# Performance work log

Hardware: AMD Instinct MI355X
Metric: run time of the kernel (lower is better)

The kernel has to match this reference:

```python
import jax, jax.numpy as jnp
import numpy as np
from jax.tree_util import tree_map

B, T, D = 2, 4096, 1024
C = 512            # chunk_size
P = 16             # n_persistent
H = 2048           # neural-memory hidden
FFN = 4 * D        # ffn_mult * d_model
LR, BETA, ALPHA = 0.01, 0.9, 0.01   # memory lr / momentum / decay
EPS_LN = 1e-5


def _l2norm(x):
    n = jnp.sqrt(jnp.sum(x * x, axis=-1, keepdims=True))
    return x / jnp.maximum(n, 1e-12)


def _ln(x, g, b):
    m = jnp.mean(x, axis=-1, keepdims=True)
    v = jnp.mean((x - m) ** 2, axis=-1, keepdims=True)
    return (x - m) * jax.lax.rsqrt(v + EPS_LN) * g + b


def _mem_mlp(mem, x):
    h = jax.nn.silu(x @ mem['w0'] + mem['b0'])
    return h @ mem['w1'] + mem['b1']


def setup_inputs() -> dict:
    key = jax.random.key(0)
    ks = iter(jax.random.split(key, 32))
    w = lambda *s: jax.random.normal(next(ks), s, jnp.float32) * 0.02
    return dict(
        x=jax.random.normal(next(ks), (B, T, D), jnp.float32),
        wq_ctx=w(D, D), wq=w(D, D), wk=w(D, D), wv=w(D, D),
        w_attn_out=w(D, D), w_gate=w(D, D),
        gate_g=jnp.ones(D), gate_b=jnp.zeros(D),
        n1_g=jnp.ones(D), n1_b=jnp.zeros(D),
        n2_g=jnp.ones(D), n2_b=jnp.zeros(D),
        ffn_w1=w(D, FFN), ffn_b1=jnp.zeros(FFN),
        ffn_w2=w(FFN, D), ffn_b2=jnp.zeros(D),
        pers=w(P, D),
        mem_w0=w(D, H), mem_b0=jnp.zeros(H),
        mem_w1=w(H, D), mem_b1=jnp.zeros(D),
        mem_wk=w(D, D), mem_wv=w(D, D),
    )


def reference(x, wq_ctx, wq, wk, wv, w_attn_out, w_gate, gate_g, gate_b,
              n1_g, n1_b, n2_g, n2_b, ffn_w1, ffn_b1, ffn_w2, ffn_b2,
              pers, mem_w0, mem_b0, mem_w1, mem_b1, mem_wk, mem_wv):
    Bv, Tv, Dv = x.shape
    n_chunks = Tv // C
    scale = Dv ** 0.5
    S = P + 2 * C   # persistent + retrieved-memory tokens + segment
    # prefix-aware causal mask: i attends to j if j < P (persistent prefix) or j <= i
    ii = jnp.arange(S)[:, None]
    jj = jnp.arange(S)[None, :]
    mask = (jj < P) | (jj <= ii)                      # (S, S)

    mem0 = dict(w0=mem_w0, b0=mem_b0, w1=mem_w1, b1=mem_b1)
    mom0 = tree_map(jnp.zeros_like, mem0)

    def attn(seq):                                    # cosine causal attention, single head
        q = _l2norm(seq @ wq) * scale
        k = _l2norm(seq @ wk)
        v = seq @ wv
        scores = jnp.einsum('bqd,bkd->bqk', q, k)
        scores = jnp.where(mask, scores, -jnp.inf)
        a = jax.nn.softmax(scores, axis=-1)
        return jnp.einsum('bqk,bkd->bqd', a, v) @ w_attn_out

    def step(carry, seg):                             # seg: (B, C, D)
        mem, mom = carry
        h = _mem_mlp(mem, _l2norm(seg @ wq_ctx))      # memory retrieval, (B, C, D)
        aug = jnp.concatenate(
            [jnp.broadcast_to(pers, (Bv, P, Dv)), h, seg], axis=1)  # (B, S, D)
        y_aug = aug + attn(_ln(aug, n1_g, n1_b))
        y_t = y_aug[:, P + C:, :]                     # strip persistent, keep last C

        # surprise-gradient memory update with momentum + decay
        kk = y_t @ mem_wk
        vv = y_t @ mem_wv
        loss = lambda m: 0.5 * jnp.sum((_mem_mlp(m, kk) - vv) ** 2) / (Bv * C)
        g = jax.grad(loss)(mem)
        mom = tree_map(lambda m_, g_: BETA * m_ + g_, mom, g)
        mem = tree_map(lambda p_, m_: (1.0 - ALPHA) * p_ - LR * m_, mem, mom)

        mem_out = _mem_mlp(mem, _l2norm(y_t @ wq_ctx))
        gate = jax.nn.sigmoid(_ln(y_t, gate_g, gate_b) @ w_gate)
        o = y_t * gate + mem_out * (1.0 - gate)
        h2 = _ln(o, n2_g, n2_b)
        o = o + (jax.nn.silu(h2 @ ffn_w1 + ffn_b1) @ ffn_w2 + ffn_b2)
        return (mem, mom), o

    x_chunks = x.reshape(Bv, n_chunks, C, Dv).transpose(1, 0, 2, 3)
    _, outs = jax.lax.scan(step, (mem0, mom0), x_chunks)   # (n_chunks, B, C, D)
    return outs.transpose(1, 0, 2, 3).reshape(Bv, Tv, Dv)
```

## Files before the change

kernel.cpp:

```cpp
#include <hip/hip_runtime.h>

#define DD 1024
#define HH 2048
#define TT 4096
#define CC 512
#define PPc 16
#define SB 1040
#define KA 1088
#define FFd 4096
#define NCH 8

typedef _Float16 f16x8 __attribute__((ext_vector_type(8)));
typedef float f32x4 __attribute__((ext_vector_type(4)));

typedef const __attribute__((address_space(1))) _Float16* gas_t;
typedef __attribute__((address_space(3))) _Float16* las_t;

__device__ __forceinline__ void async_cp16(const _Float16* g, _Float16* l) {
    __builtin_amdgcn_global_load_lds((gas_t)g, (las_t)l, 16, 0, 0);
}

template<int N> __device__ __forceinline__ void waitvm() {
    static_assert(N == 0 || N == 2 || N == 3 || N == 4 || N == 6 || N == 8, "unsupported vmcnt");
    if constexpr (N == 0)      asm volatile("s_waitcnt vmcnt(0)" ::: "memory");
    else if constexpr (N == 2) asm volatile("s_waitcnt vmcnt(2)" ::: "memory");
    else if constexpr (N == 3) asm volatile("s_waitcnt vmcnt(3)" ::: "memory");
    else if constexpr (N == 4) asm volatile("s_waitcnt vmcnt(4)" ::: "memory");
    else if constexpr (N == 6) asm volatile("s_waitcnt vmcnt(6)" ::: "memory");
    else                       asm volatile("s_waitcnt vmcnt(8)" ::: "memory");
}
#define BARRIER() asm volatile("s_barrier" ::: "memory")

struct GP {
    const _Float16* A; long bsA;
    const _Float16* Bt; long bsB;
    const float* bias;
    const float* resid; long ldr, bsR;
    const float* aux;   long ldx, bsX;
    float* Cf; long ldc, bsC;
    _Float16* Ch; long ldh, bsH;
    _Float16* Ct; long ldt, bsT;
    float* Mom;
    float* Cf2;
    float s1, s2;
    int M, N, K, act;
};

template<int BM, int BN>
__global__ __launch_bounds__(256) void gemm16(GP g)
{
    constexpr int WM = BM / 2, WN = BN / 2;
    constexpr int FA = WM / 16, FB = WN / 16;
    constexpr int LA = BM / 32, LB = BN / 32;
    constexpr int LL = LA + LB;
    constexpr int APAN = BM * 64, BPAN = BN * 64;
    constexpr int NB = 4;
    __shared__ _Float16 smem[NB * (APAN + BPAN)];
    const int tid = threadIdx.x;

    const int gx = gridDim.x, gy = gridDim.y;
    const int nwg = gx * gy * (int)gridDim.z;
    const int orig = ((int)blockIdx.z * gy + (int)blockIdx.y) * gx + (int)blockIdx.x;
    const int xcd = orig & 7, loc = orig >> 3;
    const int q8 = nwg >> 3, r8 = nwg & 7;
    const int lid = (xcd < r8 ? xcd * (q8 + 1) : r8 * (q8 + 1) + (xcd - r8) * q8) + loc;
    const int bxi = lid % gx;
    const int rem = lid / gx;
    const int byi = rem % gy;
    const int z = rem / gy;

    const int K = g.K;
    const int m0 = byi * BM, n0 = bxi * BN;
    const _Float16* Ab = g.A + (long)z * g.bsA + (long)m0 * K;
    const _Float16* Bb = g.Bt + (long)z * g.bsB + (long)n0 * K;
    const int wave = tid >> 6, lane = tid & 63;
    const int wr = wave >> 1, wc = wave & 1;
    const int fr = lane & 15, kq = lane >> 4;
    const int srow = tid >> 3;
    const int sc8 = (((tid & 7) ^ (srow & 7)) << 3);
    f32x4 acc[FA][FB] = {};

    auto stage = [&](int q, int kk) {
#pragma unroll
        for (int r = 0; r < LA; ++r)
            async_cp16(Ab + (long)(r * 32 + srow) * K + kk + sc8,
                       &smem[q * APAN + r * 2048 + wave * 512]);
#pragma unroll
        for (int r = 0; r < LB; ++r)
            async_cp16(Bb + (long)(r * 32 + srow) * K + kk + sc8,
                       &smem[NB * APAN + q * BPAN + r * 2048 + wave * 512]);
    };

    const int sl0 = ((kq ^ (fr & 7)) << 3);
    const int sl1 = (((4 + kq) ^ (fr & 7)) << 3);

    auto compute = [&](int q) {
        f16x8 af[2][FA], bf[2][FB];
        const int abase = q * APAN;
#pragma unroll
        for (int i = 0; i < FA; ++i) {
            const int ro = (wr * WM + i * 16 + fr) * 64;
            af[0][i] = *(const f16x8*)&smem[abase + ro + sl0];
            af[1][i] = *(const f16x8*)&smem[abase + ro + sl1];
        }
        const int bbase = NB * APAN + q * BPAN;
#pragma unroll
        for (int j = 0; j < FB; ++j) {
            const int ro = (wc * WN + j * 16 + fr) * 64;
            bf[0][j] = *(const f16x8*)&smem[bbase + ro + sl0];
            bf[1][j] = *(const f16x8*)&smem[bbase + ro + sl1];
        }
        __builtin_amdgcn_s_setprio(1);
#pragma unroll
        for (int h = 0; h < 2; ++h)
#pragma unroll
            for (int i = 0; i < FA; ++i)
#pragma unroll
                for (int j = 0; j < FB; ++j)
                    acc[i][j] = __builtin_amdgcn_mfma_f32_16x16x32_f16(af[h][i], bf[h][j], acc[i][j], 0, 0, 0);
        __builtin_amdgcn_s_setprio(0);
    };

    const int nk = K >> 6;
    stage(0, 0); stage(1, 64); stage(2, 128);
    int qc = 0, qs = 3;
    for (int t = 0; t < nk; ++t) {
        if (t + 2 < nk)      waitvm<2 * LL>();
        else if (t + 1 < nk) waitvm<LL>();
        else                 waitvm<0>();
        BARRIER();
        if (t + 3 < nk) stage(qs, (t + 3) << 6);
        compute(qc);
        qc = (qc + 1) & 3;
        qs = (qs + 1) & 3;
    }

#pragma unroll
    for (int i = 0; i < FA; ++i) {
        const int gm0 = m0 + wr * WM + i * 16 + kq * 4;
#pragma unroll
        for (int j = 0; j < FB; ++j) {
            const int gn = n0 + wc * WN + j * 16 + fr;
            if (gn >= g.N) continue;
            if (g.act == 4) {
                const int seg = gn >> 10, gl = gn & 1023;
#pragma unroll
                for (int r = 0; r < 4; ++r) {
                    const int gm = gm0 + r;
                    if (gm >= g.M) continue;
                    const float v = acc[i][j][r];
                    if (seg == 0) g.Ch[(long)gm * 1024 + gl] = (_Float16)v;
                    else if (seg == 1) g.Cf[(long)gm * 1024 + gl] = v;
                    else g.Cf2[(long)gm * 1024 + gl] = v;
                }
            } else {
                const float bv = g.bias ? g.bias[gn] : 0.f;
#pragma unroll
                for (int r = 0; r < 4; ++r) {
                    const int gm = gm0 + r;
                    if (gm >= g.M) continue;
                    const float raw = acc[i][j][r] + bv;
                    float av = raw;
                    if (g.act == 1) av = raw / (1.f + __expf(-raw));
                    else if (g.act == 2) {
                        const float a = g.aux[(long)z * g.bsX + (long)gm * g.ldx + gn];
                        const float s = 1.f / (1.f + __expf(-a));
                        av = raw * (s * (1.f + a * (1.f - s)));
                    }
                    float v = g.s1 * av;
                    if (g.resid) v += g.s2 * g.resid[(long)z * g.bsR + (long)gm * g.ldr + gn];
                    if (g.Cf) g.Cf[(long)z * g.bsC + (long)gm * g.ldc + gn] = (g.act == 1) ? raw : v;
                    if (g.Ch) g.Ch[(long)z * g.bsH + (long)gm * g.ldh + gn] = (_Float16)v;
                    acc[i][j][r] = v;
                }
            }
        }
    }

    if (g.Ct && (g.act != 4 || n0 < 1024)) {
        constexpr int TP = BM + 8;
        __syncthreads();
#pragma unroll
        for (int i = 0; i < FA; ++i) {
            const int lm = wr * WM + i * 16 + kq * 4;
#pragma unroll
            for (int j = 0; j < FB; ++j) {
                const int ln = wc * WN + j * 16 + fr;
#pragma unroll
                for (int r = 0; r < 4; ++r)
                    smem[ln * TP + lm + r] = (_Float16)acc[i][j][r];
            }
        }
        __syncthreads();
        constexpr int TPC = 256 / BN;
        constexpr int SEG = BM / TPC;
        const int ln = tid / TPC, part = tid % TPC;
        const int gn = n0 + ln;
        if (gn < g.N) {
            const int gmb = m0 + part * SEG;
            _Float16* dst = g.Ct + (long)z * g.bsT + (long)gn * g.ldt + gmb;
            const _Float16* src = &smem[ln * TP + part * SEG];
#pragma unroll
            for (int gi = 0; gi < SEG / 8; ++gi)
                if (gmb + gi * 8 < g.M)
                    *(uint4*)(dst + gi * 8) = *(const uint4*)(src + gi * 8);
        }
    }
}

__global__ void momupT_k(const float* __restrict__ dW1, float* __restrict__ mom1,
                         float* __restrict__ w1m, _Float16* __restrict__ w1row,
                         _Float16* __restrict__ w1t,
                         const float* __restrict__ dW0, float* __restrict__ mom0,
                         float* __restrict__ w0m, _Float16* __restrict__ w0t)
{
    __shared__ _Float16 t[64][65];
    const int b = blockIdx.x;
    const int tid = threadIdx.x;
    const float* dW; float* mom; float* wm; _Float16* wrow; _Float16* wT;
    int C, RT, r0, c0;
    if (b < 512) {
        dW = dW1; mom = mom1; wm = w1m; wrow = w1row; wT = w1t;
        C = 1024; RT = 2048;
        r0 = (b >> 4) << 6; c0 = (b & 15) << 6;
    } else {
        const int bb = b - 512;
        dW = dW0; mom = mom0; wm = w0m; wrow = nullptr; wT = w0t;
        C = 2048; RT = 1024;
        r0 = (bb >> 5) << 6; c0 = (bb & 31) << 6;
    }
#pragma unroll
    for (int i = 0; i < 4; ++i) {
        const int f = i * 256 + tid;
        const int rr = f >> 4;
        const int c4 = (f & 15) << 2;
        const long idx = (long)(r0 + rr) * C + c0 + c4;
        const float4 d = *(const float4*)(dW + idx);
        float4 mo = *(const float4*)(mom + idx);
        float4 w  = *(const float4*)(wm + idx);
        mo.x = 0.9f * mo.x + d.x; mo.y = 0.9f * mo.y + d.y;
        mo.z = 0.9f * mo.z + d.z; mo.w = 0.9f * mo.w + d.w;
        w.x = 0.99f * w.x - 0.01f * mo.x; w.y = 0.99f * w.y - 0.01f * mo.y;
        w.z = 0.99f * w.z - 0.01f * mo.z; w.w = 0.99f * w.w - 0.01f * mo.w;
        *(float4*)(mom + idx) = mo;
        *(float4*)(wm + idx) = w;
        const _Float16 h0 = (_Float16)w.x, h1 = (_Float16)w.y,
                       h2 = (_Float16)w.z, h3 = (_Float16)w.w;
        if (wrow) {
            wrow[idx] = h0; wrow[idx + 1] = h1;
            wrow[idx + 2] = h2; wrow[idx + 3] = h3;
        }
        t[rr][c4] = h0; t[rr][c4 + 1] = h1; t[rr][c4 + 2] = h2; t[rr][c4 + 3] = h3;
    }
    __syncthreads();
#pragma unroll
    for (int i = 0; i < 4; ++i) {
        const int f = i * 256 + tid;
        const int cc = f >> 4;
        const int rr4 = (f & 15) << 2;
        ushort4 u;
        u.x = *(const unsigned short*)&t[rr4][cc];
        u.y = *(const unsigned short*)&t[rr4 + 1][cc];
        u.z = *(const unsigned short*)&t[rr4 + 2][cc];
        u.w = *(const unsigned short*)&t[rr4 + 3][cc];
        *(ushort4*)(wT + (long)(c0 + cc) * RT + r0 + rr4) = u;
    }
}

__global__ void cvt_k(const float* __restrict__ in, _Float16* __restrict__ out, long n)
{
    long i = ((long)blockIdx.x * 256 + threadIdx.x) * 4;
    if (i >= n) return;
    const float4 v = *(const float4*)(in + i);
    out[i] = (_Float16)v.x; out[i + 1] = (_Float16)v.y;
    out[i + 2] = (_Float16)v.z; out[i + 3] = (_Float16)v.w;
}

__global__ void cvtT_k(const float* __restrict__ in, _Float16* __restrict__ out, int R, int C)
{
    __shared__ _Float16 t[64][65];
    const int c0 = blockIdx.x * 64, r0 = blockIdx.y * 64;
    const int tid = threadIdx.x;
    for (int i = 0; i < 16; ++i) {
        const int lin = i * 256 + tid;
        const int r = lin >> 6, cc = lin & 63;
        t[r][cc] = (_Float16)in[(long)(r0 + r) * C + c0 + cc];
    }
    __syncthreads();
    for (int i = 0; i < 16; ++i) {
        const int lin = i * 256 + tid;
        const int r2 = lin >> 6, c2 = lin & 63;
        out[(long)(c0 + r2) * R + r0 + c2] = t[c2][r2];
    }
}

__global__ void l2n16s_k(const float* __restrict__ in, long ld,
                         _Float16* __restrict__ out, float scale)
{
    const long row = blockIdx.x;
    const float* p = in + row * ld;
    _Float16* q = out + row * DD;
    const int t = threadIdx.x;
    float e0 = p[t], e1 = p[t + 256], e2 = p[t + 512], e3 = p[t + 768];
    __shared__ float rq[256];
    rq[t] = e0 * e0 + e1 * e1 + e2 * e2 + e3 * e3;
    __syncthreads();
    for (int k = 128; k; k >>= 1) { if (t < k) rq[t] += rq[t + k]; __syncthreads(); }
    const float f = scale / fmaxf(sqrtf(rq[0]), 1e-12f);
    q[t] = (_Float16)(e0 * f); q[t + 256] = (_Float16)(e1 * f);
    q[t + 512] = (_Float16)(e2 * f); q[t + 768] = (_Float16)(e3 * f);
}

__global__ void l2qk_k(const float* __restrict__ qk, _Float16* __restrict__ q16,
                       _Float16* __restrict__ k16)
{
    const int blk = blockIdx.x;
    const float* p; _Float16* o; float scale;
    if (blk < 1024) {
        const int b = blk >> 9, r = blk & 511;
        p = qk + (long)(b * SB + PPc + CC + r) * 2048;
        o = q16 + (long)blk * DD; scale = 32.f;
    } else {
        const int row = blk - 1024;
        p = qk + (long)row * 2048 + 1024;
        o = k16 + (long)row * DD; scale = 1.f;
    }
    const int t = threadIdx.x;
    float e0 = p[t], e1 = p[t + 256], e2 = p[t + 512], e3 = p[t + 768];
    __shared__ float rq[256];
    rq[t] = e0 * e0 + e1 * e1 + e2 * e2 + e3 * e3;
    __syncthreads();
    for (int k = 128; k; k >>= 1) { if (t < k) rq[t] += rq[t + k]; __syncthreads(); }
    const float f = scale / fmaxf(sqrtf(rq[0]), 1e-12f);
    o[t] = (_Float16)(e0 * f); o[t + 256] = (_Float16)(e1 * f);
    o[t + 512] = (_Float16)(e2 * f); o[t + 768] = (_Float16)(e3 * f);
}

__global__ void lnaug_k(const float* __restrict__ x, const float* __restrict__ pers,
                        const float* __restrict__ h, const float* __restrict__ g,
                        const float* __restrict__ b, _Float16* __restrict__ out, int c)
{
    const int row = blockIdx.x;
    const int bb = row / SB, i = row % SB;
    const float* p;
    if (i < PPc) p = pers + (long)i * DD;
    else if (i < PPc + CC) p = h + (long)(bb * CC + i - PPc) * DD;
    else p = x + (long)(bb * TT + c * CC + (i - PPc - CC)) * DD;
    _Float16* q = out + (long)row * DD;
    const int t = threadIdx.x;
    float e0 = p[t], e1 = p[t + 256], e2 = p[t + 512], e3 = p[t + 768];
    __shared__ float rs[256], rq[256];
    rs[t] = e0 + e1 + e2 + e3;
    rq[t] = e0 * e0 + e1 * e1 + e2 * e2 + e3 * e3;
    __syncthreads();
    for (int k = 128; k; k >>= 1) {
        if (t < k) { rs[t] += rs[t + k]; rq[t] += rq[t + k]; }
        __syncthreads();
    }
    const float mean = rs[0] * (1.f / DD);
    const float inv = rsqrtf(rq[0] * (1.f / DD) - mean * mean + 1e-5f);
    q[t]       = (_Float16)((e0 - mean) * inv * g[t]       + b[t]);
    q[t + 256] = (_Float16)((e1 - mean) * inv * g[t + 256] + b[t + 256]);
    q[t + 512] = (_Float16)((e2 - mean) * inv * g[t + 512] + b[t + 512]);
    q[t + 768] = (_Float16)((e3 - mean) * inv * g[t + 768] + b[t + 768]);
}

__global__ void softmax16_k(const float* __restrict__ sc, _Float16* __restrict__ pr)
{
    const int blk = blockIdx.x;
    const int r = blk & 511;
    const int i = PPc + CC + r;
    const float* p = sc + (long)blk * SB;
    _Float16* q = pr + (long)blk * KA;
    const int t = threadIdx.x;
    __shared__ float red[256];
    float mx = -3.0e38f;
    for (int j = t; j < SB; j += 256)
        if (j <= i) mx = fmaxf(mx, p[j]);
    red[t] = mx; __syncthreads();
    for (int k = 128; k; k >>= 1) { if (t < k) red[t] = fmaxf(red[t], red[t + k]); __syncthreads(); }
    mx = red[0]; __syncthreads();
    float sum = 0.f;
    for (int j = t; j < SB; j += 256)
        if (j <= i) sum += __expf(p[j] - mx);
    red[t] = sum; __syncthreads();
    for (int k = 128; k; k >>= 1) { if (t < k) red[t] += red[t + k]; __syncthreads(); }
    const float inv = 1.f / red[0];
    for (int j = t; j < KA; j += 256) {
        float e = 0.f;
        if (j < SB && j <= i) e = __expf(p[j] - mx) * inv;
        q[j] = (_Float16)e;
    }
}

__global__ void gateln2_k(const float* __restrict__ yt, const float* __restrict__ gp,
                          const float* __restrict__ mo, const float* __restrict__ g,
                          const float* __restrict__ b, float* __restrict__ OF,
                          _Float16* __restrict__ o16)
{
    const long row = blockIdx.x;
    const int t = threadIdx.x;
    float e[4];
    __shared__ float rs[256], rq[256];
    float ssum = 0.f, qsum = 0.f;
#pragma unroll
    for (int k = 0; k < 4; ++k) {
        const long idx = row * DD + t + k * 256;
        const float s = 1.f / (1.f + __expf(-gp[idx]));
        e[k] = yt[idx] * s + mo[idx] * (1.f - s);
        OF[idx] = e[k];
        ssum += e[k]; qsum += e[k] * e[k];
    }
    rs[t] = ssum; rq[t] = qsum;
    __syncthreads();
    for (int k = 128; k; k >>= 1) {
        if (t < k) { rs[t] += rs[t + k]; rq[t] += rq[t + k]; }
        __syncthreads();
    }
    const float mean = rs[0] * (1.f / DD);
    const float inv = rsqrtf(rq[0] * (1.f / DD) - mean * mean + 1e-5f);
#pragma unroll
    for (int k = 0; k < 4; ++k) {
        const int cc = t + k * 256;
        o16[row * DD + cc] = (_Float16)((e[k] - mean) * inv * g[cc] + b[cc]);
    }
}

__global__ void tailfuse_k(const _Float16* __restrict__ rT, const _Float16* __restrict__ daT,
                           float* __restrict__ mb0, float* __restrict__ mob0,
                           float* __restrict__ mb1, float* __restrict__ mob1,
                           const float* __restrict__ qmp, _Float16* __restrict__ qm16,
                           const float* __restrict__ ytf, const float* __restrict__ gg,
                           const float* __restrict__ gb, _Float16* __restrict__ gl)
{
    const int blk = blockIdx.x;
    const int t = threadIdx.x;
    __shared__ float rs[256], rq[256];
    if (blk < 3072) {
        const _Float16* p = (blk < 1024) ? rT + (long)blk * 1024
                                         : daT + (long)(blk - 1024) * 1024;
        rs[t] = (float)p[t] + (float)p[t + 256] + (float)p[t + 512] + (float)p[t + 768];
        __syncthreads();
        for (int k = 128; k; k >>= 1) { if (t < k) rs[t] += rs[t + k]; __syncthreads(); }
        if (t == 0) {
            const float d = rs[0];
            if (blk < 1024) {
                const float m = 0.9f * mob1[blk] + d;
                mob1[blk] = m;
                mb1[blk] = 0.99f * mb1[blk] - 0.01f * m;
            } else {
                const int j = blk - 1024;
                const float m = 0.9f * mob0[j] + d;
                mob0[j] = m;
                mb0[j] = 0.99f * mb0[j] - 0.01f * m;
            }
        }
    } else if (blk < 4096) {
        const long row = blk - 3072;
        const float* p = qmp + row * DD;
        _Float16* q = qm16 + row * DD;
        float e0 = p[t], e1 = p[t + 256], e2 = p[t + 512], e3 = p[t + 768];
        rq[t] = e0 * e0 + e1 * e1 + e2 * e2 + e3 * e3;
        __syncthreads();
        for (int k = 128; k; k >>= 1) { if (t < k) rq[t] += rq[t + k]; __syncthreads(); }
        const float f = 1.f / fmaxf(sqrtf(rq[0]), 1e-12f);
        q[t] = (_Float16)(e0 * f); q[t + 256] = (_Float16)(e1 * f);
        q[t + 512] = (_Float16)(e2 * f); q[t + 768] = (_Float16)(e3 * f);
    } else {
        const long row = blk - 4096;
        const float* p = ytf + row * DD;
        _Float16* q = gl + row * DD;
        float e0 = p[t], e1 = p[t + 256], e2 = p[t + 512], e3 = p[t + 768];
        rs[t] = e0 + e1 + e2 + e3;
        rq[t] = e0 * e0 + e1 * e1 + e2 * e2 + e3 * e3;
        __syncthreads();
        for (int k = 128; k; k >>= 1) {
            if (t < k) { rs[t] += rs[t + k]; rq[t] += rq[t + k]; }
            __syncthreads();
        }
        const float mean = rs[0] * (1.f / DD);
        const float inv = rsqrtf(rq[0] * (1.f / DD) - mean * mean + 1e-5f);
        q[t]       = (_Float16)((e0 - mean) * inv * gg[t]       + gb[t]);
        q[t + 256] = (_Float16)((e1 - mean) * inv * gg[t + 256] + gb[t + 256]);
        q[t + 512] = (_Float16)((e2 - mean) * inv * gg[t + 512] + gb[t + 512]);
        q[t + 768] = (_Float16)((e3 - mean) * inv * gg[t + 768] + gb[t + 768]);
    }
}

__global__ void zero_k(float* __restrict__ p, long n)
{
    long i = (long)blockIdx.x * 256 + threadIdx.x;
    const long st = (long)gridDim.x * 256;
    for (; i < n; i += st) p[i] = 0.f;
}

extern "C" void kernel_launch(void* const* d_in, const int* in_sizes, int n_in,
                              void* d_out, int out_size, void* d_ws, size_t ws_size,
                              hipStream_t stream)
{
    const float* x          = (const float*)d_in[0];
    const float* wq_ctx     = (const float*)d_in[1];
    const float* wq         = (const float*)d_in[2];
    const float* wk         = (const float*)d_in[3];
    const float* wv         = (const float*)d_in[4];
    const float* w_attn_out = (const float*)d_in[5];
    const float* w_gate     = (const float*)d_in[6];
    const float* gate_g     = (const float*)d_in[7];
    const float* gate_b     = (const float*)d_in[8];
    const float* n1_g       = (const float*)d_in[9];
    const float* n1_b       = (const float*)d_in[10];
    const float* n2_g       = (const float*)d_in[11];
    const float* n2_b       = (const float*)d_in[12];
    const float* ffn_w1     = (const float*)d_in[13];
    const float* ffn_b1     = (const float*)d_in[14];
    const float* ffn_w2     = (const float*)d_in[15];
    const float* ffn_b2     = (const float*)d_in[16];
    const float* pers       = (const float*)d_in[17];
    const float* mem_w0_in  = (const float*)d_in[18];
    const float* mem_b0_in  = (const float*)d_in[19];
    const float* mem_w1_in  = (const float*)d_in[20];
    const float* mem_b1_in  = (const float*)d_in[21];
    const float* mem_wk     = (const float*)d_in[22];
    const float* mem_wv     = (const float*)d_in[23];
    float* out = (float*)d_out;
    (void)in_sizes; (void)n_in; (void)out_size; (void)ws_size;

    char* cur = (char*)d_ws;
    auto allocF = [&](size_t n) { float* p = (float*)cur; cur += n * 4; return p; };
    auto allocH = [&](size_t n) { _Float16* p = (_Float16*)cur; cur += n * 2; return p; };

    float* mw0   = allocF((size_t)DD * HH);
    float* mw1   = allocF((size_t)HH * DD);
    float* mb0   = allocF(HH);
    float* mb1   = allocF(DD);
    float* mom   = allocF((size_t)DD * HH * 2 + HH + DD);
    float* mom_w0 = mom, *mom_w1 = mom + (size_t)DD * HH;
    float* mom_b0 = mom_w1 + (size_t)HH * DD, *mom_b1 = mom_b0 + HH;
    float* F32A  = allocF((size_t)1024 * DD);
    float* F32B  = allocF((size_t)1024 * DD);
    float* F32C  = allocF((size_t)1024 * HH);
    float* F32QK = allocF((size_t)2112 * 2048);
    float* YTF   = allocF((size_t)1024 * DD);
    float* OF    = allocF((size_t)1024 * DD);

    _Float16* x16    = allocH((size_t)2 * TT * DD);
    _Float16* wqcT   = allocH((size_t)DD * DD);
    _Float16* wqkT   = allocH((size_t)2048 * DD);
    _Float16* wvT    = allocH((size_t)DD * DD);
    _Float16* waoT   = allocH((size_t)DD * DD);
    _Float16* wgT    = allocH((size_t)DD * DD);
    _Float16* wmixT  = allocH((size_t)3072 * DD);
    _Float16* f1T    = allocH((size_t)FFd * DD);
    _Float16* f2T    = allocH((size_t)DD * FFd);
    _Float16* w0T    = allocH((size_t)HH * DD);
    _Float16* w1T    = allocH((size_t)DD * HH);
    _Float16* w1p    = allocH((size_t)HH * DD);
    _Float16* xn16   = allocH((size_t)1024 * DD);
    _Float16* h116   = allocH((size_t)1024 * HH);
    _Float16* laug16 = allocH((size_t)2208 * DD);
    _Float16* q16    = allocH((size_t)1024 * DD);
    _Float16* k16    = allocH((size_t)2208 * DD);
    _Float16* vT16   = allocH((size_t)2 * DD * KA);
    _Float16* pr16   = allocH((size_t)2 * 512 * KA);
    _Float16* ao16   = allocH((size_t)1024 * DD);
    _Float16* yt16   = allocH((size_t)1024 * DD);
    _Float16* kk16   = allocH((size_t)1024 * DD);
    _Float16* kkT16  = allocH((size_t)DD * 1024);
    _Float16* hs16   = allocH((size_t)1024 * HH);
    _Float16* hsT16  = allocH((size_t)HH * 1024);
    _Float16* r16    = allocH((size_t)1024 * DD);
    _Float16* rT16   = allocH((size_t)DD * 1024);
    _Float16* da0T   = allocH((size_t)HH * 1024);
    _Float16* qm16   = allocH((size_t)1024 * DD);
    _Float16* a216   = allocH((size_t)1024 * HH);
    _Float16* gl16   = allocH((size_t)1024 * DD);
    _Float16* h216   = allocH((size_t)1024 * DD);
    _Float16* f116   = allocH((size_t)1024 * FFd);

    auto launch = [&](int nz, const GP& g) {
        dim3 grid((g.N + 63) / 64, (g.M + 63) / 64, nz);
        gemm16<64, 64><<<grid, 256, 0, stream>>>(g);
    };

    hipMemcpyAsync(mw0, mem_w0_in, sizeof(float) * DD * HH, hipMemcpyDeviceToDevice, stream);
    hipMemcpyAsync(mw1, mem_w1_in, sizeof(float) * HH * DD, hipMemcpyDeviceToDevice, stream);
    hipMemcpyAsync(mb0, mem_b0_in, sizeof(float) * HH, hipMemcpyDeviceToDevice, stream);
    hipMemcpyAsync(mb1, mem_b1_in, sizeof(float) * DD, hipMemcpyDeviceToDevice, stream);
    zero_k<<<4096, 256, 0, stream>>>(mom, (long)DD * HH * 2 + HH + DD);
    cvt_k<<<(2 * TT * DD) / 1024, 256, 0, stream>>>(x, x16, (long)2 * TT * DD);
    auto T64 = [&](const float* in, _Float16* o, int R, int C) {
        cvtT_k<<<dim3(C / 64, R / 64), 256, 0, stream>>>(in, o, R, C);
    };
    T64(wq_ctx, wqcT, DD, DD);
    T64(wq, wqkT, DD, DD); T64(wk, wqkT + (size_t)1024 * DD, DD, DD);
    T64(wv, wvT, DD, DD); T64(w_attn_out, waoT, DD, DD); T64(w_gate, wgT, DD, DD);
    T64(mem_wk, wmixT, DD, DD); T64(mem_wv, wmixT + (size_t)1024 * DD, DD, DD);
    T64(wq_ctx, wmixT + (size_t)2048 * DD, DD, DD);
    T64(ffn_w1, f1T, DD, FFd); T64(ffn_w2, f2T, FFd, DD);
    T64(mem_w0_in, w0T, DD, HH); T64(mem_w1_in, w1T, HH, DD);
    cvt_k<<<(HH * DD) / 1024, 256, 0, stream>>>(mem_w1_in, w1p, (long)HH * DD);

    for (int c = 0; c < NCH; ++c) {
        GP g;
        g = GP{}; g.A = x16 + (long)c * CC * DD; g.bsA = (long)TT * DD; g.Bt = wqcT;
        g.Cf = F32A; g.ldc = DD; g.bsC = (long)CC * DD;
        g.s1 = 1.f; g.M = CC; g.N = DD; g.K = DD;
        launch(2, g);
        l2n16s_k<<<1024, 256, 0, stream>>>(F32A, DD, xn16, 1.f);
        g = GP{}; g.A = xn16; g.Bt = w0T; g.bias = mb0; g.Ch = h116; g.ldh = HH;
        g.s1 = 1.f; g.M = 1024; g.N = HH; g.K = DD; g.act = 1;
        launch(1, g);
        g = GP{}; g.A = h116; g.Bt = w1T; g.bias = mb1; g.Cf = F32B; g.ldc = DD;
        g.s1 = 1.f; g.M = 1024; g.N = DD; g.K = HH;
        launch(1, g);
        lnaug_k<<<2 * SB, 256, 0, stream>>>(x, pers, F32B, n1_g, n1_b, laug16, c);
        g = GP{}; g.A = laug16; g.Bt = wqkT; g.Cf = F32QK; g.ldc = 2048;
        g.s1 = 1.f; g.M = 2 * SB; g.N = 2048; g.K = DD;
        launch(1, g);
        l2qk_k<<<3104, 256, 0, stream>>>(F32QK, q16, k16);
        g = GP{}; g.A = laug16; g.bsA = (long)SB * DD; g.Bt = wvT;
        g.Ct = vT16; g.ldt = KA; g.bsT = (long)DD * KA;
        g.s1 = 1.f; g.M = SB; g.N = DD; g.K = DD;
        launch(2, g);
        g = GP{}; g.A = q16; g.bsA = (long)512 * DD; g.Bt = k16; g.bsB = (long)SB * DD;
        g.Cf = F32C; g.ldc = SB; g.bsC = (long)512 * SB;
        g.s1 = 1.f; g.M = 512; g.N = SB; g.K = DD;
        launch(2, g);
        softmax16_k<<<1024, 256, 0, stream>>>(F32C, pr16);
        g = GP{}; g.A = pr16; g.bsA = (long)512 * KA; g.Bt = vT16; g.bsB = (long)DD * KA;
        g.Ch = ao16; g.ldh = DD; g.bsH = (long)512 * DD;
        g.s1 = 1.f; g.M = 512; g.N = DD; g.K = KA;
        launch(2, g);
        g = GP{}; g.A = ao16; g.bsA = (long)512 * DD; g.Bt = waoT;
        g.resid = x + (long)c * CC * DD; g.ldr = DD; g.bsR = (long)TT * DD;
        g.Cf = YTF; g.ldc = DD; g.bsC = (long)512 * DD;
        g.Ch = yt16; g.ldh = DD; g.bsH = (long)512 * DD;
        g.s1 = 1.f; g.s2 = 1.f; g.M = 512; g.N = DD; g.K = DD;
        launch(2, g);
        g = GP{}; g.A = yt16; g.Bt = wmixT; g.Ch = kk16; g.Ct = kkT16; g.ldt = 1024;
        g.Cf = F32B; g.Cf2 = F32A;
        g.s1 = 1.f; g.M = 1024; g.N = 3072; g.K = DD; g.act = 4;
        launch(1, g);
        g = GP{}; g.A = kk16; g.Bt = w0T; g.bias = mb0; g.Cf = F32C; g.ldc = HH;
        g.Ch = hs16; g.ldh = HH; g.Ct = hsT16; g.ldt = 1024;
        g.s1 = 1.f; g.M = 1024; g.N = HH; g.K = DD; g.act = 1;
        launch(1, g);
        g = GP{}; g.A = hs16; g.Bt = w1T; g.bias = mb1;
        g.resid = F32B; g.ldr = DD;
        g.Ch = r16; g.ldh = DD; g.Ct = rT16; g.ldt = 1024;
        g.s1 = 1.f / 1024.f; g.s2 = -1.f / 1024.f; g.M = 1024; g.N = DD; g.K = HH;
        launch(1, g);
        g = GP{}; g.A = r16; g.Bt = w1p; g.aux = F32C; g.ldx = HH;
        g.Ct = da0T; g.ldt = 1024;
        g.s1 = 1.f; g.M = 1024; g.N = HH; g.K = DD; g.act = 2;
        launch(1, g);
        tailfuse_k<<<5120, 256, 0, stream>>>(rT16, da0T, mb0, mom_b0, mb1, mom_b1,
                                             F32A, qm16, YTF, gate_g, gate_b, gl16);
        g = GP{}; g.A = hsT16; g.Bt = rT16; g.Cf = F32C; g.ldc = DD;
        g.s1 = 1.f; g.M = HH; g.N = DD; g.K = 1024;
        launch(1, g);
        g = GP{}; g.A = kkT16; g.Bt = da0T; g.Cf = F32QK; g.ldc = HH;
        g.s1 = 1.f; g.M = DD; g.N = HH; g.K = 1024;
        launch(1, g);
        momupT_k<<<1024, 256, 0, stream>>>(F32C, mom_w1, mw1, w1p, w1T,
                                           F32QK, mom_w0, mw0, w0T);
        g = GP{}; g.A = qm16; g.Bt = w0T; g.bias = mb0; g.Ch = a216; g.ldh = HH;
        g.s1 = 1.f; g.M = 1024; g.N = HH; g.K = DD; g.act = 1;
        launch(1, g);
        g = GP{}; g.A = a216; g.Bt = w1T; g.bias = mb1; g.Cf = F32B; g.ldc = DD;
        g.s1 = 1.f; g.M = 1024; g.N = DD; g.K = HH;
        launch(1, g);
        g = GP{}; g.A = gl16; g.Bt = wgT; g.Cf = F32C; g.ldc = DD;
        g.s1 = 1.f; g.M = 1024; g.N = DD; g.K = DD;
        launch(1, g);
        gateln2_k<<<1024, 256, 0, stream>>>(YTF, F32C, F32B, n2_g, n2_b, OF, h216);
        g = GP{}; g.A = h216; g.Bt = f1T; g.bias = ffn_b1; g.Ch = f116; g.ldh = FFd;
        g.s1 = 1.f; g.M = 1024; g.N = FFd; g.K = DD; g.act = 1;
        launch(1, g);
        g = GP{}; g.A = f116; g.bsA = (long)512 * FFd; g.Bt = f2T; g.bias = ffn_b2;
        g.resid = OF; g.ldr = DD; g.bsR = (long)512 * DD;
        g.Cf = out + (long)c * CC * DD; g.ldc = DD; g.bsC = (long)TT * DD;
        g.s1 = 1.f; g.s2 = 1.f; g.M = 512; g.N = DD; g.K = FFd;
        launch(2, g);
    }
}
```

Measured before the change: 3.272 ms.

## Split-K small GEMMs with reduction fused into consumers, trim GEMM pipeline to 3 stages

Adds leading-dimension fields to the GEMM so K can be split across the z grid dimension. The two memory-MLP second-layer GEMMs (K=2048) and the gate GEMM (K=1024) now run as 2-way split-K into separate scratch buffers. The partial sums and bias are added in the downstream lnaug and gateln2 kernels, which raises occupancy for these 1024x1024 outputs. The GEMM's shared-memory ring also drops from 4 to 3 stages, cutting LDS use and possibly raising occupancy, at the cost of less prefetch depth. It also relies on the F32QK scratch being free at these points in the schedule.

```diff
diff --git a/kernel.cpp b/kernel.cpp
--- a/kernel.cpp
+++ b/kernel.cpp
@@ -32,8 +32,8 @@
 #define BARRIER() asm volatile("s_barrier" ::: "memory")
 
 struct GP {
-    const _Float16* A; long bsA;
-    const _Float16* Bt; long bsB;
+    const _Float16* A; long bsA, ldA;
+    const _Float16* Bt; long bsB, ldB;
     const float* bias;
     const float* resid; long ldr, bsR;
     const float* aux;   long ldx, bsX;
@@ -54,7 +54,7 @@
     constexpr int LA = BM / 32, LB = BN / 32;
     constexpr int LL = LA + LB;
     constexpr int APAN = BM * 64, BPAN = BN * 64;
-    constexpr int NB = 4;
+    constexpr int NB = 3;
     __shared__ _Float16 smem[NB * (APAN + BPAN)];
     const int tid = threadIdx.x;
 
@@ -70,9 +70,10 @@
     const int z = rem / gy;
 
     const int K = g.K;
+    const long ldA = g.ldA, ldB = g.ldB;
     const int m0 = byi * BM, n0 = bxi * BN;
-    const _Float16* Ab = g.A + (long)z * g.bsA + (long)m0 * K;
-    const _Float16* Bb = g.Bt + (long)z * g.bsB + (long)n0 * K;
+    const _Float16* Ab = g.A + (long)z * g.bsA + (long)m0 * ldA;
+    const _Float16* Bb = g.Bt + (long)z * g.bsB + (long)n0 * ldB;
     const int wave = tid >> 6, lane = tid & 63;
     const int wr = wave >> 1, wc = wave & 1;
     const int fr = lane & 15, kq = lane >> 4;
@@ -83,11 +84,11 @@
     auto stage = [&](int q, int kk) {
 #pragma unroll
         for (int r = 0; r < LA; ++r)
-            async_cp16(Ab + (long)(r * 32 + srow) * K + kk + sc8,
+            async_cp16(Ab + (long)(r * 32 + srow) * ldA + kk + sc8,
                        &smem[q * APAN + r * 2048 + wave * 512]);
 #pragma unroll
         for (int r = 0; r < LB; ++r)
-            async_cp16(Bb + (long)(r * 32 + srow) * K + kk + sc8,
+            async_cp16(Bb + (long)(r * 32 + srow) * ldB + kk + sc8,
                        &smem[NB * APAN + q * BPAN + r * 2048 + wave * 512]);
     };
 
@@ -122,17 +123,15 @@
     };
 
     const int nk = K >> 6;
-    stage(0, 0); stage(1, 64); stage(2, 128);
-    int qc = 0, qs = 3;
+    stage(0, 0); stage(1, 64);
+    int qc = 0, qs = 2;
     for (int t = 0; t < nk; ++t) {
-        if (t + 2 < nk)      waitvm<2 * LL>();
-        else if (t + 1 < nk) waitvm<LL>();
-        else                 waitvm<0>();
+        if (t + 1 < nk) waitvm<LL>(); else waitvm<0>();
         BARRIER();
-        if (t + 3 < nk) stage(qs, (t + 3) << 6);
+        if (t + 2 < nk) stage(qs, (t + 2) << 6);
         compute(qc);
-        qc = (qc + 1) & 3;
-        qs = (qs + 1) & 3;
+        qc = (qc == NB - 1) ? 0 : qc + 1;
+        qs = (qs == NB - 1) ? 0 : qs + 1;
     }
 
 #pragma unroll
@@ -337,18 +336,30 @@
 }
 
 __global__ void lnaug_k(const float* __restrict__ x, const float* __restrict__ pers,
-                        const float* __restrict__ h, const float* __restrict__ g,
-                        const float* __restrict__ b, _Float16* __restrict__ out, int c)
+                        const float* __restrict__ h, const float* __restrict__ h2,
+                        const float* __restrict__ hb,
+                        const float* __restrict__ g, const float* __restrict__ b,
+                        _Float16* __restrict__ out, int c)
 {
     const int row = blockIdx.x;
     const int bb = row / SB, i = row % SB;
     const float* p;
+    const float* p2 = nullptr;
     if (i < PPc) p = pers + (long)i * DD;
-    else if (i < PPc + CC) p = h + (long)(bb * CC + i - PPc) * DD;
+    else if (i < PPc + CC) {
+        const long off = (long)(bb * CC + i - PPc) * DD;
+        p = h + off; p2 = h2 + off;
+    }
     else p = x + (long)(bb * TT + c * CC + (i - PPc - CC)) * DD;
     _Float16* q = out + (long)row * DD;
     const int t = threadIdx.x;
     float e0 = p[t], e1 = p[t + 256], e2 = p[t + 512], e3 = p[t + 768];
+    if (p2) {
+        e0 += p2[t]       + hb[t];
+        e1 += p2[t + 256] + hb[t + 256];
+        e2 += p2[t + 512] + hb[t + 512];
+        e3 += p2[t + 768] + hb[t + 768];
+    }
     __shared__ float rs[256], rq[256];
     rs[t] = e0 + e1 + e2 + e3;
     rq[t] = e0 * e0 + e1 * e1 + e2 * e2 + e3 * e3;
@@ -393,10 +404,12 @@
     }
 }
 
-__global__ void gateln2_k(const float* __restrict__ yt, const float* __restrict__ gp,
-                          const float* __restrict__ mo, const float* __restrict__ g,
-                          const float* __restrict__ b, float* __restrict__ OF,
-                          _Float16* __restrict__ o16)
+__global__ void gateln2_k(const float* __restrict__ yt,
+                          const float* __restrict__ gp, const float* __restrict__ gp2,
+                          const float* __restrict__ mo, const float* __restrict__ mo2,
+                          const float* __restrict__ mb,
+                          const float* __restrict__ g, const float* __restrict__ b,
+                          float* __restrict__ OF, _Float16* __restrict__ o16)
 {
     const long row = blockIdx.x;
     const int t = threadIdx.x;
@@ -405,9 +418,12 @@
     float ssum = 0.f, qsum = 0.f;
 #pragma unroll
     for (int k = 0; k < 4; ++k) {
-        const long idx = row * DD + t + k * 256;
-        const float s = 1.f / (1.f + __expf(-gp[idx]));
-        e[k] = yt[idx] * s + mo[idx] * (1.f - s);
+        const int cc = t + k * 256;
+        const long idx = row * DD + cc;
+        const float gv = gp[idx] + gp2[idx];
+        const float mv = mo[idx] + mo2[idx] + mb[cc];
+        const float s = 1.f / (1.f + __expf(-gv));
+        e[k] = yt[idx] * s + mv * (1.f - s);
         OF[idx] = e[k];
         ssum += e[k]; qsum += e[k] * e[k];
     }
@@ -577,7 +593,12 @@
     _Float16* h216   = allocH((size_t)1024 * DD);
     _Float16* f116   = allocH((size_t)1024 * FFd);
 
-    auto launch = [&](int nz, const GP& g) {
+    float* SPL0 = F32QK;
+    float* SPL1 = F32QK + (size_t)1024 * 1024;
+
+    auto launch = [&](int nz, GP g) {
+        if (!g.ldA) g.ldA = g.K;
+        if (!g.ldB) g.ldB = g.K;
         dim3 grid((g.N + 63) / 64, (g.M + 63) / 64, nz);
         gemm16<64, 64><<<grid, 256, 0, stream>>>(g);
     };
@@ -610,10 +631,12 @@
         g = GP{}; g.A = xn16; g.Bt = w0T; g.bias = mb0; g.Ch = h116; g.ldh = HH;
         g.s1 = 1.f; g.M = 1024; g.N = HH; g.K = DD; g.act = 1;
         launch(1, g);
-        g = GP{}; g.A = h116; g.Bt = w1T; g.bias = mb1; g.Cf = F32B; g.ldc = DD;
-        g.s1 = 1.f; g.M = 1024; g.N = DD; g.K = HH;
-        launch(1, g);
-        lnaug_k<<<2 * SB, 256, 0, stream>>>(x, pers, F32B, n1_g, n1_b, laug16, c);
+        g = GP{}; g.A = h116; g.bsA = 1024; g.ldA = HH;
+        g.Bt = w1T; g.bsB = 1024; g.ldB = HH;
+        g.Cf = F32B; g.ldc = DD; g.bsC = (long)(SPL0 - F32B);
+        g.s1 = 1.f; g.M = 1024; g.N = DD; g.K = 1024;
+        launch(2, g);
+        lnaug_k<<<2 * SB, 256, 0, stream>>>(x, pers, F32B, SPL0, mb1, n1_g, n1_b, laug16, c);
         g = GP{}; g.A = laug16; g.Bt = wqkT; g.Cf = F32QK; g.ldc = 2048;
         g.s1 = 1.f; g.M = 2 * SB; g.N = 2048; g.K = DD;
         launch(1, g);
@@ -667,13 +690,18 @@
         g = GP{}; g.A = qm16; g.Bt = w0T; g.bias = mb0; g.Ch = a216; g.ldh = HH;
         g.s1 = 1.f; g.M = 1024; g.N = HH; g.K = DD; g.act = 1;
         launch(1, g);
-        g = GP{}; g.A = a216; g.Bt = w1T; g.bias = mb1; g.Cf = F32B; g.ldc = DD;
-        g.s1 = 1.f; g.M = 1024; g.N = DD; g.K = HH;
-        launch(1, g);
-        g = GP{}; g.A = gl16; g.Bt = wgT; g.Cf = F32C; g.ldc = DD;
-        g.s1 = 1.f; g.M = 1024; g.N = DD; g.K = DD;
-        launch(1, g);
-        gateln2_k<<<1024, 256, 0, stream>>>(YTF, F32C, F32B, n2_g, n2_b, OF, h216);
+        g = GP{}; g.A = a216; g.bsA = 1024; g.ldA = HH;
+        g.Bt = w1T; g.bsB = 1024; g.ldB = HH;
+        g.Cf = F32B; g.ldc = DD; g.bsC = (long)(SPL0 - F32B);
+        g.s1 = 1.f; g.M = 1024; g.N = DD; g.K = 1024;
+        launch(2, g);
+        g = GP{}; g.A = gl16; g.bsA = 512; g.ldA = DD;
+        g.Bt = wgT; g.bsB = 512; g.ldB = DD;
+        g.Cf = F32C; g.ldc = DD; g.bsC = (long)(SPL1 - F32C);
+        g.s1 = 1.f; g.M = 1024; g.N = DD; g.K = 512;
+        launch(2, g);
+        gateln2_k<<<1024, 256, 0, stream>>>(YTF, F32C, SPL1, F32B, SPL0, mb1,
+                                            n2_g, n2_b, OF, h216);
         g = GP{}; g.A = h216; g.Bt = f1T; g.bias = ffn_b1; g.Ch = f116; g.ldh = FFd;
         g.s1 = 1.f; g.M = 1024; g.N = FFd; g.K = DD; g.act = 1;
         launch(1, g);
```

After: 3.039 ms. 1.08x faster.
